# Optimization experiments

Hardware: AMD Instinct MI355X
Metric: run time of the kernel (lower is better)

Reference implementation:

```python
import jax, jax.numpy as jnp
import numpy as np

N = 50000      # nodes
E = 800000     # directed edges
D = 128        # in_dim == vertex_embed_dim
L = 3          # num_layers
EPS = 1e-5     # BatchNorm eps


def setup_inputs() -> dict:
    key = jax.random.key(0)
    k0, k1, k2 = jax.random.split(key, 3)
    x = jax.random.normal(k0, (N, D), dtype=jnp.float32)
    edge_index = jax.random.randint(k1, (2, E), 0, N, dtype=jnp.int32)
    Ws = jax.random.normal(k2, (L, D, D), dtype=jnp.float32) * 0.05
    bs = jnp.zeros((L, D), dtype=jnp.float32)
    gammas = jnp.ones((L, D), dtype=jnp.float32)
    betas = jnp.zeros((L, D), dtype=jnp.float32)
    return {"x": x, "edge_index": edge_index, "Ws": Ws, "bs": bs,
            "gammas": gammas, "betas": betas}


def reference(x, edge_index, Ws, bs, gammas, betas):
    # --- GCN normalization with self-loops (computed once, shared by all layers) ---
    loop = jnp.arange(N, dtype=edge_index.dtype)
    src = jnp.concatenate([edge_index[0], loop])   # [E+N]
    dst = jnp.concatenate([edge_index[1], loop])   # [E+N]
    deg = jax.ops.segment_sum(jnp.ones_like(dst, dtype=x.dtype), dst,
                              num_segments=N)       # in-degree of A + I
    dinv = jnp.where(deg > 0, jax.lax.rsqrt(deg), 0.0)
    norm = (dinv[src] * dinv[dst])[:, None]         # [E+N, 1]

    o = x
    h_v = [o]
    for i in range(L):
        h = o @ Ws[i]                                         # linear (no bias)
        msg = h[src] * norm                                   # gather + scale
        agg = jax.ops.segment_sum(msg, dst, num_segments=N)   # scatter-add
        agg = agg + bs[i]                                     # GCNConv bias
        # BatchNorm1d (training mode, biased batch stats)
        mu = jnp.mean(agg, axis=0)
        var = jnp.var(agg, axis=0)
        o = jax.nn.relu(gammas[i] * (agg - mu) * jax.lax.rsqrt(var + EPS)
                        + betas[i])
        h_v.append(o)
    return jnp.concatenate(h_v, axis=1)   # JK concat: [N, D*(L+1)]
```

## Files before the change

### kernel.cpp

```cpp
#include <hip/hip_runtime.h>


#define EPS_BN 1e-5f
#define NPW 4

typedef short short8v __attribute__((ext_vector_type(8)));
typedef float float4v __attribute__((ext_vector_type(4)));

__device__ __forceinline__ unsigned bf16rne(float f){
  unsigned x = __float_as_uint(f);
  return (x + 0x7fffu + ((x >> 16) & 1u)) >> 16;
}
__device__ __forceinline__ float bflo(unsigned q){ return __uint_as_float(q << 16); }
__device__ __forceinline__ float bfhi(unsigned q){ return __uint_as_float(q & 0xffff0000u); }

__global__ void k_zero_i32(int* __restrict__ p, int n){
  int i = blockIdx.x*256 + threadIdx.x;
  if (i < n) p[i] = 0;
}

__global__ void k_count(const int* __restrict__ dst, int* __restrict__ cnt, int E){
  int i = blockIdx.x*256 + threadIdx.x;
  if (i < E) atomicAdd(&cnt[dst[i]], 1);
}

__global__ void k_scan1(const int* __restrict__ cnt, int* __restrict__ out,
                        int* __restrict__ blksum, float* __restrict__ dinv, int n){
  __shared__ int sh[256];
  int t = threadIdx.x;
  int base = blockIdx.x*1024 + t*4;
  int v[4];
  #pragma unroll
  for (int j=0;j<4;j++){
    int raw = (base+j < n) ? cnt[base+j] : 0;
    if (base+j < n) dinv[base+j] = rsqrtf((float)raw + 1.0f);
    v[j] = (base+j < n) ? ((raw + 7) & ~7) : 0;
  }
  int tsum = v[0]+v[1]+v[2]+v[3];
  sh[t] = tsum;
  __syncthreads();
  #pragma unroll
  for (int off=1; off<256; off<<=1){
    int x = (t>=off) ? sh[t-off] : 0;
    __syncthreads();
    sh[t] += x;
    __syncthreads();
  }
  if (t==255) blksum[blockIdx.x] = sh[255];
  int run = sh[t] - tsum;
  #pragma unroll
  for (int j=0;j<4;j++){ if (base+j < n) out[base+j] = run; run += v[j]; }
}

__global__ void k_scan3(int* __restrict__ out, int* __restrict__ rowcur,
                        const int* __restrict__ blksum, int nscan,
                        const int* __restrict__ cnt, int2* __restrict__ colpk, int n){
  __shared__ int lb[64];
  int t = threadIdx.x;
  if (t < nscan) lb[t] = blksum[t];
  __syncthreads();
  int i = blockIdx.x*256 + t;
  int myblk = i >> 10;
  int pre = 0, tot = 0;
  for (int k=0;k<nscan;k++){ int bv = lb[k]; tot += bv; if (k < myblk) pre += bv; }
  if (i < n){
    int r = out[i] + pre;
    out[i] = r;
    rowcur[i] = r;
    int c = cnt[i];
    int pc = (c + 7) & ~7;
    for (int p = r + c; p < r + pc; p++) colpk[p] = make_int2(0, 0);
  }
  if (i == 0) out[n] = tot;
}

__global__ void k_fill(const int* __restrict__ src, const int* __restrict__ dst,
                       const float* __restrict__ dinv,
                       int* __restrict__ rowcur, int2* __restrict__ colpk, int E){
  int e = blockIdx.x*256 + threadIdx.x;
  if (e < E){
    int d = dst[e];
    int pos = atomicAdd(&rowcur[d], 1);
    int s = src[e];
    colpk[pos] = make_int2(s, __float_as_int(dinv[s]));
  }
}

template<int MODE>
__launch_bounds__(256)
__global__ void k_gemm(const void* __restrict__ Av, const float* __restrict__ W,
                       const float* __restrict__ statrep,
                       const float* __restrict__ gamma, const float* __restrict__ beta,
                       float* __restrict__ out, int colOff, unsigned* __restrict__ H2,
                       int n){
  __shared__ unsigned short Al[64*128];
  __shared__ unsigned short Wt[128*128];
  __shared__ float ssL[256];
  const int t = threadIdx.x;

  if constexpr (MODE == 1){
    if (t < 128){
      float s = 0.f, s2 = 0.f;
      #pragma unroll
      for (int r=0;r<8;r++){
        s  += statrep[r*256 + t];
        s2 += statrep[r*256 + 128 + t];
      }
      float invn = 1.0f / (float)n;
      float mu  = s * invn;
      float var = s2 * invn - mu*mu;
      float rs  = rsqrtf(var + EPS_BN);
      float sc  = gamma[t] * rs;
      ssL[t]       = sc;
      ssL[128 + t] = beta[t] - mu * sc;
    }
    __syncthreads();
  }

  {
    int row = t >> 2;
    int q   = t & 3;
    int grow = blockIdx.x*64 + row;
    int gr  = grow > n-1 ? n-1 : grow;
    unsigned short* dstb = Al + row*128;
    int swz = (row & 7) << 3;
    if constexpr (MODE == 0){
      const float4* src = (const float4*)((const float*)Av + (size_t)gr*128 + q*32);
      #pragma unroll
      for (int c8=0; c8<4; c8++){
        float4 f0 = src[c8*2], f1 = src[c8*2+1];
        if (grow < n){
          float4* op = (float4*)(out + (size_t)grow*512 + q*32 + c8*8);
          op[0] = f0; op[1] = f1;
        }
        uint4 pk;
        pk.x = bf16rne(f0.x) | (bf16rne(f0.y)<<16);
        pk.y = bf16rne(f0.z) | (bf16rne(f0.w)<<16);
        pk.z = bf16rne(f1.x) | (bf16rne(f1.y)<<16);
        pk.w = bf16rne(f1.z) | (bf16rne(f1.w)<<16);
        int ke = q*32 + c8*8;
        *(uint4*)(dstb + (ke ^ swz)) = pk;
      }
    } else {
      const uint4* src = (const uint4*)((const unsigned*)Av + (size_t)gr*64 + q*16);
      #pragma unroll
      for (int c8=0; c8<4; c8++){
        uint4 ld = src[c8];
        int k0 = q*32 + c8*8;
        float4 o0, o1;
        o0.x = fmaxf(fmaf(bflo(ld.x), ssL[k0+0], ssL[128+k0+0]), 0.f);
        o0.y = fmaxf(fmaf(bfhi(ld.x), ssL[k0+1], ssL[128+k0+1]), 0.f);
        o0.z = fmaxf(fmaf(bflo(ld.y), ssL[k0+2], ssL[128+k0+2]), 0.f);
        o0.w = fmaxf(fmaf(bfhi(ld.y), ssL[k0+3], ssL[128+k0+3]), 0.f);
        o1.x = fmaxf(fmaf(bflo(ld.z), ssL[k0+4], ssL[128+k0+4]), 0.f);
        o1.y = fmaxf(fmaf(bfhi(ld.z), ssL[k0+5], ssL[128+k0+5]), 0.f);
        o1.z = fmaxf(fmaf(bflo(ld.w), ssL[k0+6], ssL[128+k0+6]), 0.f);
        o1.w = fmaxf(fmaf(bfhi(ld.w), ssL[k0+7], ssL[128+k0+7]), 0.f);
        if (grow < n){
          float4* op = (float4*)(out + (size_t)grow*512 + colOff + k0);
          op[0] = o0; op[1] = o1;
        }
        uint4 pk;
        pk.x = bf16rne(o0.x) | (bf16rne(o0.y)<<16);
        pk.y = bf16rne(o0.z) | (bf16rne(o0.w)<<16);
        pk.z = bf16rne(o1.x) | (bf16rne(o1.y)<<16);
        pk.w = bf16rne(o1.z) | (bf16rne(o1.w)<<16);
        *(uint4*)(dstb + (k0 ^ swz)) = pk;
      }
    }
  }
  {
    int nn = t & 127;
    int kh = t >> 7;
    int swz = (nn & 7) << 3;
    unsigned short* dstb = Wt + nn*128;
    #pragma unroll 4
    for (int i=0;i<32;i++){
      int k = (i*2 + kh)*2;
      float w0 = W[(size_t)k*128 + nn];
      float w1 = W[(size_t)(k+1)*128 + nn];
      *(unsigned*)(dstb + (k ^ swz)) = bf16rne(w0) | (bf16rne(w1)<<16);
    }
  }
  __syncthreads();

  const int w  = t >> 6;
  const int l  = t & 63;
  const int lo = l & 15, hi = l >> 4;

  const unsigned short* arow = Al + (w*16 + lo)*128;
  const int aswz = ((w*16 + lo) & 7) << 3;
  short8v a[4];
  #pragma unroll
  for (int kc=0;kc<4;kc++){
    int ke = kc*32 + hi*8;
    a[kc] = *(const short8v*)(arow + (ke ^ aswz));
  }

  float4v acc[8];
  #pragma unroll
  for (int ct=0;ct<8;ct++) acc[ct] = (float4v)(0.f);

  #pragma unroll
  for (int ct=0;ct<8;ct++){
    int col = ct*16 + lo;
    const unsigned short* brow = Wt + col*128;
    int bswz = (col & 7) << 3;
    #pragma unroll
    for (int kc=0;kc<4;kc++){
      int ke = kc*32 + hi*8;
      short8v b = *(const short8v*)(brow + (ke ^ bswz));
      acc[ct] = __builtin_amdgcn_mfma_f32_16x16x32_bf16(a[kc], b, acc[ct], 0, 0, 0);
    }
  }

  const int rbase = blockIdx.x*64 + w*16;
  #pragma unroll
  for (int ct=0;ct<8;ct++){
    int col = ct*16 + lo;
    #pragma unroll
    for (int r=0;r<4;r++){
      unsigned bits  = bf16rne(acc[ct][r]);
      unsigned other = (unsigned)__shfl_xor((int)bits, 1, 64);
      int grow = rbase + hi*4 + r;
      if (!(l & 1) && grow < n)
        H2[(size_t)grow*64 + (col>>1)] = bits | (other<<16);
    }
  }
}

__launch_bounds__(256)
__global__ void k_agg(const unsigned* __restrict__ h2, const int* __restrict__ rowptr,
                      const int4* __restrict__ colpk4, const float* __restrict__ dinv,
                      unsigned* __restrict__ aggsc,
                      float* __restrict__ statrep, int n){
  __shared__ float red[4*256];
  const int lane = threadIdx.x & 63;
  const int wv   = __builtin_amdgcn_readfirstlane(threadIdx.x >> 6);
  const int v0   = (blockIdx.x*4 + wv) * NPW;
  float s0=0.f, s1=0.f, q0s=0.f, q1s=0.f;
  #pragma unroll 1
  for (int vi=0; vi<NPW; vi++){
    int v = v0 + vi;
    if (v < n){
      int j   = __builtin_amdgcn_readfirstlane(rowptr[v]);
      int end = __builtin_amdgcn_readfirstlane(rowptr[v+1]);
      unsigned qs = h2[(size_t)v*64 + lane];
      float dv = dinv[v];
      float a0 = 0.f, a1 = 0.f;
      if (j < end){
        int4 qa = colpk4[(j>>1)  ];
        int4 qb = colpk4[(j>>1)+1];
        int4 qc = colpk4[(j>>1)+2];
        int4 qd = colpk4[(j>>1)+3];
        #pragma unroll 1
        for (;;){
          int jn = j + 8;
          bool more = jn < end;
          int4 na, nb, nc, nd;
          if (more){
            na = colpk4[(jn>>1)  ];
            nb = colpk4[(jn>>1)+1];
            nc = colpk4[(jn>>1)+2];
            nd = colpk4[(jn>>1)+3];
          }
          unsigned e0=h2[(size_t)qa.x*64+lane], e1=h2[(size_t)qa.z*64+lane];
          unsigned e2=h2[(size_t)qb.x*64+lane], e3=h2[(size_t)qb.z*64+lane];
          unsigned e4=h2[(size_t)qc.x*64+lane], e5=h2[(size_t)qc.z*64+lane];
          unsigned e6=h2[(size_t)qd.x*64+lane], e7=h2[(size_t)qd.z*64+lane];
          float w0=__int_as_float(qa.y), w1=__int_as_float(qa.w);
          float w2=__int_as_float(qb.y), w3=__int_as_float(qb.w);
          float w4=__int_as_float(qc.y), w5=__int_as_float(qc.w);
          float w6=__int_as_float(qd.y), w7=__int_as_float(qd.w);
          a0 = fmaf(w0, bflo(e0), a0);  a1 = fmaf(w0, bfhi(e0), a1);
          a0 = fmaf(w1, bflo(e1), a0);  a1 = fmaf(w1, bfhi(e1), a1);
          a0 = fmaf(w2, bflo(e2), a0);  a1 = fmaf(w2, bfhi(e2), a1);
          a0 = fmaf(w3, bflo(e3), a0);  a1 = fmaf(w3, bfhi(e3), a1);
          a0 = fmaf(w4, bflo(e4), a0);  a1 = fmaf(w4, bfhi(e4), a1);
          a0 = fmaf(w5, bflo(e5), a0);  a1 = fmaf(w5, bfhi(e5), a1);
          a0 = fmaf(w6, bflo(e6), a0);  a1 = fmaf(w6, bfhi(e6), a1);
          a0 = fmaf(w7, bflo(e7), a0);  a1 = fmaf(w7, bfhi(e7), a1);
          if (!more) break;
          qa = na; qb = nb; qc = nc; qd = nd; j = jn;
        }
      }
      a0 = dv*(a0 + dv*bflo(qs));
      a1 = dv*(a1 + dv*bfhi(qs));
      aggsc[(size_t)v*64 + lane] = bf16rne(a0) | (bf16rne(a1) << 16);
      s0 += a0; q0s = fmaf(a0,a0,q0s);
      s1 += a1; q1s = fmaf(a1,a1,q1s);
    }
  }
  red[wv*256 + 2*lane]       = s0;
  red[wv*256 + 2*lane+1]     = s1;
  red[wv*256 + 128+2*lane]   = q0s;
  red[wv*256 + 128+2*lane+1] = q1s;
  __syncthreads();
  int t = threadIdx.x;
  float tot = red[t] + red[256+t] + red[512+t] + red[768+t];
  atomicAdd(&statrep[((blockIdx.x & 7)<<8) + t], tot);
}

__launch_bounds__(256)
__global__ void k_bnfinal(const unsigned* __restrict__ aggsc,
                          const float* __restrict__ statrep,
                          const float* __restrict__ gamma, const float* __restrict__ beta,
                          float* __restrict__ out, int colOff, int n){
  __shared__ float ssL[256];
  int t = threadIdx.x;
  if (t < 128){
    float s = 0.f, s2 = 0.f;
    #pragma unroll
    for (int r=0;r<8;r++){
      s  += statrep[r*256 + t];
      s2 += statrep[r*256 + 128 + t];
    }
    float invn = 1.0f / (float)n;
    float mu  = s * invn;
    float var = s2 * invn - mu*mu;
    float rs  = rsqrtf(var + EPS_BN);
    float sc  = gamma[t] * rs;
    ssL[t]       = sc;
    ssL[128 + t] = beta[t] - mu * sc;
  }
  __syncthreads();
  int i = blockIdx.x*256 + t;
  if (i >= n*16) return;
  int v = i >> 4, c = i & 15;
  uint4 ld = *(const uint4*)(aggsc + (size_t)v*64 + c*4);
  int k0 = c*8;
  float4 o0, o1;
  o0.x = fmaxf(fmaf(bflo(ld.x), ssL[k0+0], ssL[128+k0+0]), 0.f);
  o0.y = fmaxf(fmaf(bfhi(ld.x), ssL[k0+1], ssL[128+k0+1]), 0.f);
  o0.z = fmaxf(fmaf(bflo(ld.y), ssL[k0+2], ssL[128+k0+2]), 0.f);
  o0.w = fmaxf(fmaf(bfhi(ld.y), ssL[k0+3], ssL[128+k0+3]), 0.f);
  o1.x = fmaxf(fmaf(bflo(ld.z), ssL[k0+4], ssL[128+k0+4]), 0.f);
  o1.y = fmaxf(fmaf(bfhi(ld.z), ssL[k0+5], ssL[128+k0+5]), 0.f);
  o1.z = fmaxf(fmaf(bflo(ld.w), ssL[k0+6], ssL[128+k0+6]), 0.f);
  o1.w = fmaxf(fmaf(bfhi(ld.w), ssL[k0+7], ssL[128+k0+7]), 0.f);
  float4* op = (float4*)(out + (size_t)v*512 + colOff + k0);
  op[0] = o0; op[1] = o1;
}

extern "C" void kernel_launch(void* const* d_in, const int* in_sizes, int n_in,
                              void* d_out, int out_size, void* d_ws, size_t ws_size,
                              hipStream_t stream){
  const float* x      = (const float*)d_in[0];
  const int*   ei     = (const int*)d_in[1];
  const float* Ws     = (const float*)d_in[2];
  const float* gammas = (const float*)d_in[4];
  const float* betas  = (const float*)d_in[5];
  const int N = in_sizes[0] / 128;
  const int E = in_sizes[1] / 2;
  float* out = (float*)d_out;

  const int EPADCAP = E + 7*N + 8;

  char* w = (char*)d_ws;
  auto alloc = [&](size_t bytes)->char*{
    char* p = w; w += (bytes + 255) & ~(size_t)255; return p;
  };
  int*      cnt     = (int*)     alloc((size_t)N*4);
  float*    statrep = (float*)   alloc(3*8*256*4);
  int*      rowptr  = (int*)     alloc((size_t)(N+1)*4);
  int*      rowcur  = (int*)     alloc((size_t)N*4);
  int*      blksum  = (int*)     alloc(64*4);
  int2*     colpk   = (int2*)    alloc((size_t)EPADCAP*8);
  float*    dinv    = (float*)   alloc((size_t)N*4);
  unsigned* h2      = (unsigned*)alloc((size_t)N*64*4);
  unsigned* aggsc   = (unsigned*)alloc((size_t)N*64*4);

  const int* srcArr = ei;
  const int* dstArr = ei + E;

  const int nbN = (N + 255)/256;
  const int nbE = (E + 255)/256;
  const int nscan = (N + 1023)/1024;
  const int nz = (int)(((char*)statrep - (char*)cnt)/4) + 3*8*256;

  k_zero_i32<<<(nz + 255)/256,256,0,stream>>>(cnt, nz);
  k_count<<<nbE,256,0,stream>>>(dstArr, cnt, E);
  k_scan1<<<nscan,256,0,stream>>>(cnt, rowptr, blksum, dinv, N);
  k_scan3<<<nbN,256,0,stream>>>(rowptr, rowcur, blksum, nscan, cnt, colpk, N);
  k_fill<<<nbE,256,0,stream>>>(srcArr, dstArr, dinv, rowcur, colpk, E);

  const int gemmGrid = (N + 63)/64;
  const int aggGrid  = (N + 4*NPW-1)/(4*NPW);

  for (int l=0; l<3; l++){
    if (l == 0)
      k_gemm<0><<<gemmGrid,256,0,stream>>>(x, Ws, nullptr, nullptr, nullptr,
                                           out, 0, h2, N);
    else
      k_gemm<1><<<gemmGrid,256,0,stream>>>(aggsc, Ws + (size_t)l*128*128,
                                           statrep + (l-1)*2048,
                                           gammas + (l-1)*128, betas + (l-1)*128,
                                           out, l*128, h2, N);
    k_agg<<<aggGrid,256,0,stream>>>(h2, rowptr, (const int4*)colpk, dinv, aggsc,
                                    statrep + l*2048, N);
  }
  k_bnfinal<<<(N*16 + 255)/256,256,0,stream>>>(aggsc, statrep + 2*2048,
                                               gammas + 2*128, betas + 2*128,
                                               out, 3*128, N);
}
```

Baseline: 278.9 us.

## Pack CSR entries into 32-bit src+bf16 weight, fuse degree count into first GEMM

Each CSR entry now packs the 16-bit source index and a bf16 dinv weight into one int, halving adjacency traffic. The aggregation loop also prefetches the next batch of neighbour feature gathers, not just indices, to deepen memory-level parallelism. The edge-count kernel is merged into extra blocks of the layer-0 GEMM launch, and statistic replicas grow to 16 with NPW reduced to 2. Risks: the 16-bit index only holds for N below 65536, the weight loses precision, and the prefetch raises register pressure.

Measured after the change: 263.3 us. -5.6%, faster.

```diff
diff --git a/kernel.cpp b/kernel.cpp
--- a/kernel.cpp
+++ b/kernel.cpp
@@ -2,7 +2,8 @@
 
 
 #define EPS_BN 1e-5f
-#define NPW 4
+#define NPW 2
+#define REP 16
 
 typedef short short8v __attribute__((ext_vector_type(8)));
 typedef float float4v __attribute__((ext_vector_type(4)));
@@ -17,11 +18,6 @@
 __global__ void k_zero_i32(int* __restrict__ p, int n){
   int i = blockIdx.x*256 + threadIdx.x;
   if (i < n) p[i] = 0;
-}
-
-__global__ void k_count(const int* __restrict__ dst, int* __restrict__ cnt, int E){
-  int i = blockIdx.x*256 + threadIdx.x;
-  if (i < E) atomicAdd(&cnt[dst[i]], 1);
 }
 
 __global__ void k_scan1(const int* __restrict__ cnt, int* __restrict__ out,
@@ -54,7 +50,7 @@
 
 __global__ void k_scan3(int* __restrict__ out, int* __restrict__ rowcur,
                         const int* __restrict__ blksum, int nscan,
-                        const int* __restrict__ cnt, int2* __restrict__ colpk, int n){
+                        const int* __restrict__ cnt, int* __restrict__ colsrc, int n){
   __shared__ int lb[64];
   int t = threadIdx.x;
   if (t < nscan) lb[t] = blksum[t];
@@ -69,20 +65,20 @@
     rowcur[i] = r;
     int c = cnt[i];
     int pc = (c + 7) & ~7;
-    for (int p = r + c; p < r + pc; p++) colpk[p] = make_int2(0, 0);
+    for (int p = r + c; p < r + pc; p++) colsrc[p] = 0;
   }
   if (i == 0) out[n] = tot;
 }
 
 __global__ void k_fill(const int* __restrict__ src, const int* __restrict__ dst,
                        const float* __restrict__ dinv,
-                       int* __restrict__ rowcur, int2* __restrict__ colpk, int E){
+                       int* __restrict__ rowcur, int* __restrict__ colsrc, int E){
   int e = blockIdx.x*256 + threadIdx.x;
   if (e < E){
     int d = dst[e];
     int pos = atomicAdd(&rowcur[d], 1);
     int s = src[e];
-    colpk[pos] = make_int2(s, __float_as_int(dinv[s]));
+    colsrc[pos] = s | (int)(bf16rne(dinv[s]) << 16);
   }
 }
 
@@ -92,17 +88,26 @@
                        const float* __restrict__ statrep,
                        const float* __restrict__ gamma, const float* __restrict__ beta,
                        float* __restrict__ out, int colOff, unsigned* __restrict__ H2,
-                       int n){
+                       int n,
+                       const int* __restrict__ dstE, int* __restrict__ cnt, int E,
+                       int gemmGrid){
+  const int t = threadIdx.x;
+  if constexpr (MODE == 0){
+    if ((int)blockIdx.x >= gemmGrid){
+      int i = ((int)blockIdx.x - gemmGrid)*256 + t;
+      if (i < E) atomicAdd(&cnt[dstE[i]], 1);
+      return;
+    }
+  }
   __shared__ unsigned short Al[64*128];
   __shared__ unsigned short Wt[128*128];
   __shared__ float ssL[256];
-  const int t = threadIdx.x;
 
   if constexpr (MODE == 1){
     if (t < 128){
       float s = 0.f, s2 = 0.f;
       #pragma unroll
-      for (int r=0;r<8;r++){
+      for (int r=0;r<REP;r++){
         s  += statrep[r*256 + t];
         s2 += statrep[r*256 + 128 + t];
       }
@@ -229,15 +234,21 @@
   }
 }
 
+#define GATH(d) (*(const unsigned*)(h2c + (size_t)(unsigned)(((d)&0xffff)<<8) + lane4))
+#define FMA2(d,g) { float wv_=__uint_as_float((unsigned)(d)&0xffff0000u); \
+                    a0=fmaf(wv_,bflo(g),a0); a1=fmaf(wv_,bfhi(g),a1); }
 __launch_bounds__(256)
 __global__ void k_agg(const unsigned* __restrict__ h2, const int* __restrict__ rowptr,
-                      const int4* __restrict__ colpk4, const float* __restrict__ dinv,
+                      const int* __restrict__ colsrc, const float* __restrict__ dinv,
                       unsigned* __restrict__ aggsc,
                       float* __restrict__ statrep, int n){
   __shared__ float red[4*256];
-  const int lane = threadIdx.x & 63;
+  const char* h2c = (const char*)h2;
+  const int lane  = threadIdx.x & 63;
+  const unsigned lane4 = lane*4;
   const int wv   = __builtin_amdgcn_readfirstlane(threadIdx.x >> 6);
   const int v0   = (blockIdx.x*4 + wv) * NPW;
+  const int4* c4 = (const int4*)colsrc;
   float s0=0.f, s1=0.f, q0s=0.f, q1s=0.f;
   #pragma unroll 1
   for (int vi=0; vi<NPW; vi++){
@@ -245,43 +256,30 @@
     if (v < n){
       int j   = __builtin_amdgcn_readfirstlane(rowptr[v]);
       int end = __builtin_amdgcn_readfirstlane(rowptr[v+1]);
-      unsigned qs = h2[(size_t)v*64 + lane];
+      unsigned qs = *(const unsigned*)(h2c + (size_t)v*256 + lane4);
       float dv = dinv[v];
       float a0 = 0.f, a1 = 0.f;
       if (j < end){
-        int4 qa = colpk4[(j>>1)  ];
-        int4 qb = colpk4[(j>>1)+1];
-        int4 qc = colpk4[(j>>1)+2];
-        int4 qd = colpk4[(j>>1)+3];
+        int4 A0 = c4[(j>>2)], A1 = c4[(j>>2)+1];
+        unsigned g0=GATH(A0.x), g1=GATH(A0.y), g2=GATH(A0.z), g3=GATH(A0.w);
+        unsigned g4=GATH(A1.x), g5=GATH(A1.y), g6=GATH(A1.z), g7=GATH(A1.w);
         #pragma unroll 1
         for (;;){
           int jn = j + 8;
           bool more = jn < end;
-          int4 na, nb, nc, nd;
+          int4 B0, B1;
+          unsigned p0,p1,p2,p3,p4,p5,p6,p7;
           if (more){
-            na = colpk4[(jn>>1)  ];
-            nb = colpk4[(jn>>1)+1];
-            nc = colpk4[(jn>>1)+2];
-            nd = colpk4[(jn>>1)+3];
+            B0 = c4[(jn>>2)]; B1 = c4[(jn>>2)+1];
+            p0=GATH(B0.x); p1=GATH(B0.y); p2=GATH(B0.z); p3=GATH(B0.w);
+            p4=GATH(B1.x); p5=GATH(B1.y); p6=GATH(B1.z); p7=GATH(B1.w);
           }
-          unsigned e0=h2[(size_t)qa.x*64+lane], e1=h2[(size_t)qa.z*64+lane];
-          unsigned e2=h2[(size_t)qb.x*64+lane], e3=h2[(size_t)qb.z*64+lane];
-          unsigned e4=h2[(size_t)qc.x*64+lane], e5=h2[(size_t)qc.z*64+lane];
-          unsigned e6=h2[(size_t)qd.x*64+lane], e7=h2[(size_t)qd.z*64+lane];
-          float w0=__int_as_float(qa.y), w1=__int_as_float(qa.w);
-          float w2=__int_as_float(qb.y), w3=__int_as_float(qb.w);
-          float w4=__int_as_float(qc.y), w5=__int_as_float(qc.w);
-          float w6=__int_as_float(qd.y), w7=__int_as_float(qd.w);
-          a0 = fmaf(w0, bflo(e0), a0);  a1 = fmaf(w0, bfhi(e0), a1);
-          a0 = fmaf(w1, bflo(e1), a0);  a1 = fmaf(w1, bfhi(e1), a1);
-          a0 = fmaf(w2, bflo(e2), a0);  a1 = fmaf(w2, bfhi(e2), a1);
-          a0 = fmaf(w3, bflo(e3), a0);  a1 = fmaf(w3, bfhi(e3), a1);
-          a0 = fmaf(w4, bflo(e4), a0);  a1 = fmaf(w4, bfhi(e4), a1);
-          a0 = fmaf(w5, bflo(e5), a0);  a1 = fmaf(w5, bfhi(e5), a1);
-          a0 = fmaf(w6, bflo(e6), a0);  a1 = fmaf(w6, bfhi(e6), a1);
-          a0 = fmaf(w7, bflo(e7), a0);  a1 = fmaf(w7, bfhi(e7), a1);
+          FMA2(A0.x,g0) FMA2(A0.y,g1) FMA2(A0.z,g2) FMA2(A0.w,g3)
+          FMA2(A1.x,g4) FMA2(A1.y,g5) FMA2(A1.z,g6) FMA2(A1.w,g7)
           if (!more) break;
-          qa = na; qb = nb; qc = nc; qd = nd; j = jn;
+          A0=B0; A1=B1;
+          g0=p0; g1=p1; g2=p2; g3=p3; g4=p4; g5=p5; g6=p6; g7=p7;
+          j = jn;
         }
       }
       a0 = dv*(a0 + dv*bflo(qs));
@@ -298,7 +296,7 @@
   __syncthreads();
   int t = threadIdx.x;
   float tot = red[t] + red[256+t] + red[512+t] + red[768+t];
-  atomicAdd(&statrep[((blockIdx.x & 7)<<8) + t], tot);
+  atomicAdd(&statrep[((blockIdx.x & (REP-1))<<8) + t], tot);
 }
 
 __launch_bounds__(256)
@@ -311,7 +309,7 @@
   if (t < 128){
     float s = 0.f, s2 = 0.f;
     #pragma unroll
-    for (int r=0;r<8;r++){
+    for (int r=0;r<REP;r++){
       s  += statrep[r*256 + t];
       s2 += statrep[r*256 + 128 + t];
     }
@@ -361,11 +359,11 @@
     char* p = w; w += (bytes + 255) & ~(size_t)255; return p;
   };
   int*      cnt     = (int*)     alloc((size_t)N*4);
-  float*    statrep = (float*)   alloc(3*8*256*4);
+  float*    statrep = (float*)   alloc(3*REP*256*4);
   int*      rowptr  = (int*)     alloc((size_t)(N+1)*4);
   int*      rowcur  = (int*)     alloc((size_t)N*4);
   int*      blksum  = (int*)     alloc(64*4);
-  int2*     colpk   = (int2*)    alloc((size_t)EPADCAP*8);
+  int*      colsrc  = (int*)     alloc((size_t)EPADCAP*4);
   float*    dinv    = (float*)   alloc((size_t)N*4);
   unsigned* h2      = (unsigned*)alloc((size_t)N*64*4);
   unsigned* aggsc   = (unsigned*)alloc((size_t)N*64*4);
@@ -376,30 +374,30 @@
   const int nbN = (N + 255)/256;
   const int nbE = (E + 255)/256;
   const int nscan = (N + 1023)/1024;
-  const int nz = (int)(((char*)statrep - (char*)cnt)/4) + 3*8*256;
-
-  k_zero_i32<<<(nz + 255)/256,256,0,stream>>>(cnt, nz);
-  k_count<<<nbE,256,0,stream>>>(dstArr, cnt, E);
-  k_scan1<<<nscan,256,0,stream>>>(cnt, rowptr, blksum, dinv, N);
-  k_scan3<<<nbN,256,0,stream>>>(rowptr, rowcur, blksum, nscan, cnt, colpk, N);
-  k_fill<<<nbE,256,0,stream>>>(srcArr, dstArr, dinv, rowcur, colpk, E);
+  const int nz = (int)(((char*)statrep - (char*)cnt)/4) + 3*REP*256;
 
   const int gemmGrid = (N + 63)/64;
   const int aggGrid  = (N + 4*NPW-1)/(4*NPW);
 
+  k_zero_i32<<<(nz + 255)/256,256,0,stream>>>(cnt, nz);
+  k_gemm<0><<<gemmGrid + nbE,256,0,stream>>>(x, Ws, nullptr, nullptr, nullptr,
+                                             out, 0, h2, N,
+                                             dstArr, cnt, E, gemmGrid);
+  k_scan1<<<nscan,256,0,stream>>>(cnt, rowptr, blksum, dinv, N);
+  k_scan3<<<nbN,256,0,stream>>>(rowptr, rowcur, blksum, nscan, cnt, colsrc, N);
+  k_fill<<<nbE,256,0,stream>>>(srcArr, dstArr, dinv, rowcur, colsrc, E);
+
   for (int l=0; l<3; l++){
-    if (l == 0)
-      k_gemm<0><<<gemmGrid,256,0,stream>>>(x, Ws, nullptr, nullptr, nullptr,
-                                           out, 0, h2, N);
-    else
+    if (l > 0)
       k_gemm<1><<<gemmGrid,256,0,stream>>>(aggsc, Ws + (size_t)l*128*128,
-                                           statrep + (l-1)*2048,
+                                           statrep + (l-1)*REP*256,
                                            gammas + (l-1)*128, betas + (l-1)*128,
-                                           out, l*128, h2, N);
-    k_agg<<<aggGrid,256,0,stream>>>(h2, rowptr, (const int4*)colpk, dinv, aggsc,
-                                    statrep + l*2048, N);
-  }
-  k_bnfinal<<<(N*16 + 255)/256,256,0,stream>>>(aggsc, statrep + 2*2048,
+                                           out, l*128, h2, N,
+                                           nullptr, nullptr, 0, gemmGrid);
+    k_agg<<<aggGrid,256,0,stream>>>(h2, rowptr, colsrc, dinv, aggsc,
+                                    statrep + l*REP*256, N);
+  }
+  k_bnfinal<<<(N*16 + 255)/256,256,0,stream>>>(aggsc, statrep + 2*REP*256,
                                                gammas + 2*128, betas + 2*128,
                                                out, 3*128, N);
 }
```
